# Optimization experiments

Measured on AMD Instinct MI355X. Metric: run time of the kernel, lower is better.

Reference implementation:

```python
import jax, jax.numpy as jnp
import numpy as np

B, A = 1024, 256                 # batch, padded action-space size
N_ENT, N_REL = 100000, 500
E_DIM, R_DIM, H_DIM = 200, 200, 400
ACT_DIM = E_DIM + R_DIM          # action embedding = [rel_emb ; ent_emb]
IN_DIM = E_DIM + H_DIM + R_DIM   # X = cat([E, H, Q])
HUGE = 1e31                      # ops.HUGE_INT
EPS = 1e-20


def setup_inputs() -> dict:
    key = jax.random.key(0)
    ks = jax.random.split(key, 12)
    inp = {
        "e": jax.random.randint(ks[0], (B,), 0, N_ENT),
        "q": jax.random.randint(ks[1], (B,), 0, N_REL),
        "H": jax.random.normal(ks[2], (B, H_DIM), dtype=jnp.float32),
        "r_space": jax.random.randint(ks[3], (B, A), 0, N_REL),
        "e_space": jax.random.randint(ks[4], (B, A), 0, N_ENT),
        "action_mask": jax.random.randint(ks[5], (B, A), 0, 2).astype(jnp.int32),
        # learned parameters
        "entity_emb": jax.random.normal(ks[6], (N_ENT, E_DIM), dtype=jnp.float32) * 0.02,
        "relation_emb": jax.random.normal(ks[7], (N_REL, R_DIM), dtype=jnp.float32) * 0.02,
        "W1": jax.random.normal(ks[8], (IN_DIM, ACT_DIM), dtype=jnp.float32) * (1.0 / np.sqrt(IN_DIM)),
        "b1": jnp.zeros((ACT_DIM,), jnp.float32),
        "W2": jax.random.normal(ks[9], (ACT_DIM, ACT_DIM), dtype=jnp.float32) * (1.0 / np.sqrt(ACT_DIM)),
        "b2": jnp.zeros((ACT_DIM,), jnp.float32),
        "W_att": jax.random.normal(ks[10], (ACT_DIM, R_DIM), dtype=jnp.float32) * (1.0 / np.sqrt(ACT_DIM)),
        "b_att": jnp.zeros((R_DIM,), jnp.float32),
    }
    return inp


def reference(e, q, H, r_space, e_space, action_mask,
              entity_emb, relation_emb, W1, b1, W2, b2, W_att, b_att):
    # state featurization: X = cat([E, H, Q])  -> [B, IN_DIM]
    E = entity_emb[e]
    Q = relation_emb[q]
    X = jnp.concatenate([E, H, Q], axis=-1)
    X = jax.nn.relu(X @ W1 + b1)          # W1 + ReLU (dropout = identity in eval)
    X2 = X @ W2 + b2                      # [B, ACT_DIM]

    # relation attention over all relations
    relation_att = jax.nn.softmax((X2 @ W_att + b_att) @ relation_emb.T, axis=-1)  # [B, N_REL]

    # action embeddings: A = cat([rel_emb[r_space], ent_emb[e_space]])  [B, A, ACT_DIM]
    A_emb = jnp.concatenate([relation_emb[r_space], entity_emb[e_space]], axis=-1)

    mask = action_mask.astype(X2.dtype)
    scores = jnp.einsum('bad,bd->ba', A_emb, X2) - (1.0 - mask) * HUGE
    action_dist = jax.nn.softmax(scores, axis=-1)                      # [B, A]
    entropy = -jnp.sum(action_dist * jnp.log(action_dist + EPS), axis=-1)  # [B]
    return action_dist, entropy, relation_att
```

## Files before the change

### kernel.cpp

```cpp
#include <hip/hip_runtime.h>

#define BATCH   1024
#define ASZ     256
#define EDIM    200
#define RDIM    200
#define HDIM    400
#define ACTDIM  400
#define INDIM   800
#define NRELS   500

typedef __attribute__((ext_vector_type(8))) short short8v;
typedef __attribute__((ext_vector_type(4))) float float4v;
typedef unsigned short u16;

__device__ __forceinline__ u16 f2bf(float f) {
    union { float f; unsigned u; } v; v.f = f;
    unsigned r = v.u + 0x7FFFu + ((v.u >> 16) & 1u);
    return (u16)(r >> 16);
}

template<int ABF, int BBF, int CT, int GAT>
__device__ __forceinline__ void mgemm_body(
    const void* __restrict__ A, const void* __restrict__ B,
    float* __restrict__ Cp, u16* __restrict__ CTout, int ldct,
    int M, int N, int K, int bn, int bm, int z, int nz,
    const int* e_s, const int* q_s,
    const float* __restrict__ Hm, const float* __restrict__ ent,
    const float* __restrict__ rel,
    short* As, short* Bs, int t)
{
    const int tot = (K + 31) >> 5;
    const int s0 = (z * tot) / nz, s1 = ((z + 1) * tot) / nz;

    const int lane = t & 63, w = t >> 6;
    const int l15 = lane & 15, l4 = lane >> 4;
    const int wr = (w >> 1) * 32, wc = (w & 1) * 32;

    const int row = t >> 2;
    const int kc  = (t & 3) * 8;

    float4v acc00 = {0.f,0.f,0.f,0.f}, acc01 = {0.f,0.f,0.f,0.f};
    float4v acc10 = {0.f,0.f,0.f,0.f}, acc11 = {0.f,0.f,0.f,0.f};

    for (int s = s0; s < s1; ++s) {
        const int k0 = s << 5;
        {
            const int gk = k0 + kc;
            __attribute__((aligned(16))) u16 v[8];
            if (GAT) {
                const float* p;
                if (gk < EDIM)            p = ent + (long)e_s[row] * EDIM + gk;
                else if (gk < EDIM+HDIM)  p = Hm  + (long)(bm + row) * HDIM + (gk - EDIM);
                else                      p = rel + (long)q_s[row] * RDIM + (gk - EDIM - HDIM);
                float4 f0 = *(const float4*)p;
                float4 f1 = *(const float4*)(p + 4);
                v[0]=f2bf(f0.x); v[1]=f2bf(f0.y); v[2]=f2bf(f0.z); v[3]=f2bf(f0.w);
                v[4]=f2bf(f1.x); v[5]=f2bf(f1.y); v[6]=f2bf(f1.z); v[7]=f2bf(f1.w);
            } else {
                const int gr = bm + row;
                if (gr < M && gk + 8 <= K) {
                    if (ABF) {
                        *(uint4*)v = *(const uint4*)((const u16*)A + (long)gr * K + gk);
                    } else {
                        const float* p = (const float*)A + (long)gr * K + gk;
                        float4 f0 = *(const float4*)p;
                        float4 f1 = *(const float4*)(p + 4);
                        v[0]=f2bf(f0.x); v[1]=f2bf(f0.y); v[2]=f2bf(f0.z); v[3]=f2bf(f0.w);
                        v[4]=f2bf(f1.x); v[5]=f2bf(f1.y); v[6]=f2bf(f1.z); v[7]=f2bf(f1.w);
                    }
                } else {
#pragma unroll
                    for (int i = 0; i < 8; ++i) v[i] = 0;
                }
            }
            *(uint4*)&As[row * 40 + kc] = *(uint4*)v;
        }
        {
            const int gr = bn + row;
            const int gk = k0 + kc;
            __attribute__((aligned(16))) u16 v[8];
            if (gr < N && gk + 8 <= K) {
                if (BBF) {
                    *(uint4*)v = *(const uint4*)((const u16*)B + (long)gr * K + gk);
                } else {
                    const float* p = (const float*)B + (long)gr * K + gk;
                    float4 f0 = *(const float4*)p;
                    float4 f1 = *(const float4*)(p + 4);
                    v[0]=f2bf(f0.x); v[1]=f2bf(f0.y); v[2]=f2bf(f0.z); v[3]=f2bf(f0.w);
                    v[4]=f2bf(f1.x); v[5]=f2bf(f1.y); v[6]=f2bf(f1.z); v[7]=f2bf(f1.w);
                }
            } else {
#pragma unroll
                for (int i = 0; i < 8; ++i) v[i] = 0;
            }
            *(uint4*)&Bs[row * 40 + kc] = *(uint4*)v;
        }
        __syncthreads();
        short8v a0 = *(short8v*)&As[(wr      + l15) * 40 + l4 * 8];
        short8v a1 = *(short8v*)&As[(wr + 16 + l15) * 40 + l4 * 8];
        short8v b0 = *(short8v*)&Bs[(wc      + l15) * 40 + l4 * 8];
        short8v b1 = *(short8v*)&Bs[(wc + 16 + l15) * 40 + l4 * 8];
        acc00 = __builtin_amdgcn_mfma_f32_16x16x32_bf16(a0, b0, acc00, 0, 0, 0);
        acc01 = __builtin_amdgcn_mfma_f32_16x16x32_bf16(a0, b1, acc01, 0, 0, 0);
        acc10 = __builtin_amdgcn_mfma_f32_16x16x32_bf16(a1, b0, acc10, 0, 0, 0);
        acc11 = __builtin_amdgcn_mfma_f32_16x16x32_bf16(a1, b1, acc11, 0, 0, 0);
        __syncthreads();
    }

    const int rm0 = bm + wr + l4 * 4;
    const int cn0 = bn + wc + l15;
    if (CT == 1) {
        float* dst = Cp + (long)z * M * N;
#pragma unroll
        for (int r = 0; r < 4; ++r) {
            int gm0 = rm0 + r, gm1 = rm0 + 16 + r;
            if (gm0 < M) {
                if (cn0 < N)      dst[(long)gm0 * N + cn0]      = acc00[r];
                if (cn0 + 16 < N) dst[(long)gm0 * N + cn0 + 16] = acc01[r];
            }
            if (gm1 < M) {
                if (cn0 < N)      dst[(long)gm1 * N + cn0]      = acc10[r];
                if (cn0 + 16 < N) dst[(long)gm1 * N + cn0 + 16] = acc11[r];
            }
        }
    } else {
#pragma unroll
        for (int r = 0; r < 4; ++r) {
            int gm0 = rm0 + r, gm1 = rm0 + 16 + r;
            if (gm0 < M) {
                if (cn0 < N)      CTout[(long)cn0 * ldct + gm0]        = f2bf(acc00[r]);
                if (cn0 + 16 < N) CTout[(long)(cn0 + 16) * ldct + gm0] = f2bf(acc01[r]);
            }
            if (gm1 < M) {
                if (cn0 < N)      CTout[(long)cn0 * ldct + gm1]        = f2bf(acc10[r]);
                if (cn0 + 16 < N) CTout[(long)(cn0 + 16) * ldct + gm1] = f2bf(acc11[r]);
            }
        }
    }
}

template<int ABF, int BBF, int CT, int GAT>
__global__ __launch_bounds__(256) void k_mgemm(
    const void* __restrict__ A, const void* __restrict__ B,
    float* __restrict__ Cp, u16* __restrict__ CTout, int ldct,
    int M, int N, int K,
    const int* __restrict__ eidx, const int* __restrict__ qidx,
    const float* __restrict__ Hm, const float* __restrict__ ent,
    const float* __restrict__ rel)
{
    __shared__ __align__(16) short As[64 * 40];
    __shared__ __align__(16) short Bs[64 * 40];
    __shared__ int e_s[64], q_s[64];
    const int t = threadIdx.x;
    const int bm = blockIdx.y * 64;
    if (GAT) {
        if (t < 64) {
            e_s[t] = eidx[bm + t];
            q_s[t] = qidx[bm + t];
        }
        __syncthreads();
    }
    mgemm_body<ABF, BBF, CT, GAT>(A, B, Cp, CTout, ldct, M, N, K,
                                  blockIdx.x * 64, bm, blockIdx.z, gridDim.z,
                                  e_s, q_s, Hm, ent, rel, As, Bs, t);
}

__global__ __launch_bounds__(256) void k_prep_all(
    const float* __restrict__ W1, const float* __restrict__ W2,
    const float* __restrict__ batt, const float* __restrict__ rel,
    const float* __restrict__ Watt,
    u16* __restrict__ W1t, u16* __restrict__ W2t,
    u16* __restrict__ BbigT, float* __restrict__ bbig2)
{
    __shared__ __align__(16) short As[64 * 40];
    __shared__ __align__(16) short Bs[64 * 40];
    __shared__ float tile[32][33];
    __shared__ float bs[200];

    int blk = blockIdx.x, t = threadIdx.x;

    if (blk < 325) {
        int tk = blk / 13, tn = blk % 13;
        int k0 = tk * 32, n0 = tn * 32;
        int i = t >> 3, j4 = (t & 7) * 4;
#pragma unroll
        for (int jj = 0; jj < 4; ++jj) {
            int n = n0 + j4 + jj;
            tile[i][j4 + jj] = (n < 400) ? W1[(long)(k0 + i) * 400 + n] : 0.f;
        }
        __syncthreads();
        int o = t >> 3;
        if (n0 + o < 400) {
            ushort4 u;
            u.x = f2bf(tile[j4 + 0][o]); u.y = f2bf(tile[j4 + 1][o]);
            u.z = f2bf(tile[j4 + 2][o]); u.w = f2bf(tile[j4 + 3][o]);
            *(ushort4*)(W1t + (long)(n0 + o) * 800 + k0 + j4) = u;
        }
    } else if (blk < 494) {
        int idx = blk - 325;
        int tk = idx / 13, tn = idx % 13;
        int k0 = tk * 32, n0 = tn * 32;
        int i = t >> 3, j4 = (t & 7) * 4;
#pragma unroll
        for (int jj = 0; jj < 4; ++jj) {
            int n = n0 + j4 + jj;
            tile[i][j4 + jj] = (k0 + i < 400 && n < 400) ? W2[(long)(k0 + i) * 400 + n] : 0.f;
        }
        __syncthreads();
        int o = t >> 3;
        if (n0 + o < 400) {
#pragma unroll
            for (int jj = 0; jj < 4; ++jj) {
                int k = k0 + j4 + jj;
                if (k < 400) W2t[(long)(n0 + o) * 400 + k] = f2bf(tile[j4 + jj][o]);
            }
        }
    } else if (blk < 594) {
        int gid = (blk - 494) * 256 + t;
        for (int g = gid; g < 50000; g += 100 * 256) {
            int n = g / 100, kq = (g % 100) * 4;
            ushort4 u;
            u.x = (kq + 0 < 200) ? f2bf(rel[(long)n * 200 + kq + 0]) : (u16)0;
            u.y = (kq + 1 < 200) ? f2bf(rel[(long)n * 200 + kq + 1]) : (u16)0;
            u.z = (kq + 2 < 200) ? f2bf(rel[(long)n * 200 + kq + 2]) : (u16)0;
            u.w = (kq + 3 < 200) ? f2bf(rel[(long)n * 200 + kq + 3]) : (u16)0;
            *(ushort4*)(BbigT + (long)(500 + n) * 400 + kq) = u;
        }
    } else if (blk == 594) {
        if (t < 200) bs[t] = batt[t];
        __syncthreads();
        for (int n = t; n < NRELS; n += 256) {
            const float* rr = rel + (long)n * RDIM;
            float s = 0.f;
            for (int k = 0; k < 200; ++k) s += bs[k] * rr[k];
            bbig2[n] = s;
        }
    } else {
        int idx = blk - 595;
        int bn = (idx & 7) * 64, bm = (idx >> 3) * 64;
        mgemm_body<0, 0, 2, 0>(Watt, rel, nullptr, BbigT, 400,
                               400, 500, 200, bn, bm, 0, 1,
                               nullptr, nullptr, nullptr, nullptr, nullptr,
                               As, Bs, t);
    }
}

template<int RELU, int OUT>
__global__ __launch_bounds__(128) void k_reduce2(
    const float* __restrict__ Cp, const float* __restrict__ bias,
    float* __restrict__ Cf, u16* __restrict__ Cb, int M, int N, int nks)
{
    int m = blockIdx.x;
    int nf4 = N >> 2;
    for (int f = threadIdx.x; f < nf4; f += 128) {
        long off = (long)m * N + f * 4;
        float4 s = *(const float4*)(Cp + off);
        for (int ks = 1; ks < nks; ++ks) {
            float4 v = *(const float4*)(Cp + (long)ks * M * N + off);
            s.x += v.x; s.y += v.y; s.z += v.z; s.w += v.w;
        }
        float4 bb = *(const float4*)(bias + f * 4);
        s.x += bb.x; s.y += bb.y; s.z += bb.z; s.w += bb.w;
        if (RELU) {
            s.x = fmaxf(s.x, 0.f); s.y = fmaxf(s.y, 0.f);
            s.z = fmaxf(s.z, 0.f); s.w = fmaxf(s.w, 0.f);
        }
        if (OUT != 1) *(float4*)(Cf + off) = s;
        if (OUT != 0) {
            ushort4 u;
            u.x = f2bf(s.x); u.y = f2bf(s.y); u.z = f2bf(s.z); u.w = f2bf(s.w);
            *(ushort4*)(Cb + off) = u;
        }
    }
}

__global__ __launch_bounds__(512) void k_scores(
    const float* __restrict__ X2, const float* __restrict__ Cp,
    const float* __restrict__ brel,
    const int* __restrict__ r_space, const int* __restrict__ e_space,
    const int* __restrict__ amask,
    const float* __restrict__ ent_emb,
    float* __restrict__ out_dist, float* __restrict__ out_ent,
    float* __restrict__ out_rel)
{
    int b = blockIdx.x, t = threadIdx.x;
    int wave = t >> 6, lane = t & 63;
    __shared__ __align__(16) float4 xt4[50];
    __shared__ float xr[NRELS];
    __shared__ float sc[ASZ];
    __shared__ int   smask[ASZ];
    __shared__ float red[8];

    const float* rowX2 = X2 + (long)b * ACTDIM;
    const float* c0 = Cp + (long)b * 1000;
    const float* c1 = Cp + (long)BATCH * 1000 + (long)b * 1000;
    if (t < 50) xt4[t] = *(const float4*)(rowX2 + 200 + 4 * t);
    for (int i = t; i < NRELS; i += 512) xr[i] = c0[500 + i] + c1[500 + i];

    int abase = wave * 32;
    int r_idx = 0, e_idx = 0, mk = 0;
    if (lane < 32) {
        long base = (long)b * ASZ + abase + lane;
        r_idx = r_space[base];
        e_idx = e_space[base];
        mk    = amask[base];
        smask[abase + lane] = mk;
    }
    __syncthreads();

    float4 x = (lane < 50) ? xt4[lane] : make_float4(0.f, 0.f, 0.f, 0.f);

#pragma unroll
    for (int i = 0; i < 8; ++i) {
        float s[4] = {0.f, 0.f, 0.f, 0.f};
        int rj[4];
#pragma unroll
        for (int j = 0; j < 4; ++j) {
            int a = 4 * i + j;
            int m0 = __shfl(mk, a);
            rj[j]  = __shfl(r_idx, a);
            if (m0) {
                int e0 = __shfl(e_idx, a);
                if (lane < 50) {
                    float4 v = ((const float4*)(ent_emb + (long)e0 * EDIM))[lane];
                    s[j] = v.x * x.x + v.y * x.y + v.z * x.z + v.w * x.w;
                }
            }
        }
#pragma unroll
        for (int off = 32; off > 0; off >>= 1) {
            s[0] += __shfl_xor(s[0], off);
            s[1] += __shfl_xor(s[1], off);
            s[2] += __shfl_xor(s[2], off);
            s[3] += __shfl_xor(s[3], off);
        }
        if (lane == 0) {
            sc[abase + 4 * i + 0] = s[0] + xr[rj[0]];
            sc[abase + 4 * i + 1] = s[1] + xr[rj[1]];
            sc[abase + 4 * i + 2] = s[2] + xr[rj[2]];
            sc[abase + 4 * i + 3] = s[3] + xr[rj[3]];
        }
    }
    __syncthreads();

    float v = -3.4e38f;
    float evv = 0.f;
    if (t < ASZ) v = smask[t] ? sc[t] : -1e31f;

    float m = v;
#pragma unroll
    for (int off = 32; off > 0; off >>= 1) m = fmaxf(m, __shfl_xor(m, off));
    if (t < ASZ && lane == 0) red[wave] = m;
    __syncthreads();
    float mm = fmaxf(fmaxf(red[0], red[1]), fmaxf(red[2], red[3]));
    __syncthreads();

    if (t < ASZ) evv = expf(v - mm);
    float ss = evv;
#pragma unroll
    for (int off = 32; off > 0; off >>= 1) ss += __shfl_xor(ss, off);
    if (t < ASZ && lane == 0) red[wave] = ss;
    __syncthreads();
    float tot = red[0] + red[1] + red[2] + red[3];
    __syncthreads();

    float term = 0.f;
    if (t < ASZ) {
        float p = evv / tot;
        out_dist[(long)b * ASZ + t] = p;
        term = p * logf(p + 1e-20f);
    }
#pragma unroll
    for (int off = 32; off > 0; off >>= 1) term += __shfl_xor(term, off);
    if (t < ASZ && lane == 0) red[wave] = term;
    __syncthreads();
    if (t == 0) out_ent[b] = -(red[0] + red[1] + red[2] + red[3]);
    __syncthreads();

    float rv = (t < NRELS) ? (c0[t] + c1[t] + brel[t]) : -3.4e38f;

    float rm = rv;
#pragma unroll
    for (int off = 32; off > 0; off >>= 1) rm = fmaxf(rm, __shfl_xor(rm, off));
    if (lane == 0) red[wave] = rm;
    __syncthreads();
    rm = fmaxf(fmaxf(fmaxf(red[0], red[1]), fmaxf(red[2], red[3])),
               fmaxf(fmaxf(red[4], red[5]), fmaxf(red[6], red[7])));
    __syncthreads();

    float rev = (t < NRELS) ? expf(rv - rm) : 0.f;
    float rs = rev;
#pragma unroll
    for (int off = 32; off > 0; off >>= 1) rs += __shfl_xor(rs, off);
    if (lane == 0) red[wave] = rs;
    __syncthreads();
    rs = red[0] + red[1] + red[2] + red[3] + red[4] + red[5] + red[6] + red[7];
    if (t < NRELS) out_rel[(long)b * NRELS + t] = rev / rs;
}

extern "C" void kernel_launch(void* const* d_in, const int* in_sizes, int n_in,
                              void* d_out, int out_size, void* d_ws, size_t ws_size,
                              hipStream_t stream)
{
    const int*   e       = (const int*)  d_in[0];
    const int*   q       = (const int*)  d_in[1];
    const float* H       = (const float*)d_in[2];
    const int*   r_space = (const int*)  d_in[3];
    const int*   e_space = (const int*)  d_in[4];
    const int*   amask   = (const int*)  d_in[5];
    const float* ent     = (const float*)d_in[6];
    const float* rel     = (const float*)d_in[7];
    const float* W1      = (const float*)d_in[8];
    const float* b1      = (const float*)d_in[9];
    const float* W2      = (const float*)d_in[10];
    const float* b2      = (const float*)d_in[11];
    const float* Watt    = (const float*)d_in[12];
    const float* batt    = (const float*)d_in[13];

    float* out      = (float*)d_out;
    float* out_dist = out;
    float* out_ent  = out + (long)BATCH * ASZ;
    float* out_rel  = out_ent + BATCH;

    char* ws = (char*)d_ws;
    u16*   X1_bf  = (u16*)  (ws + 0);
    float* X2     = (float*)(ws + 819200);
    u16*   X2_bf  = (u16*)  (ws + 2457600);
    u16*   W1t    = (u16*)  (ws + 3276800);
    u16*   W2t    = (u16*)  (ws + 3916800);
    u16*   BbigT  = (u16*)  (ws + 4236800);
    float* bbig2  = (float*)(ws + 5036800);
    float* Cp     = (float*)(ws + 5242880);

    k_prep_all<<<651, 256, 0, stream>>>(W1, W2, batt, rel, Watt,
                                        W1t, W2t, BbigT, bbig2);

    k_mgemm<1, 1, 1, 1><<<dim3(7, 16, 4), 256, 0, stream>>>(
        nullptr, W1t, Cp, nullptr, 0, BATCH, ACTDIM, INDIM, e, q, H, ent, rel);
    k_reduce2<1, 1><<<BATCH, 128, 0, stream>>>(Cp, b1, nullptr, X1_bf, BATCH, ACTDIM, 4);

    k_mgemm<1, 1, 1, 0><<<dim3(7, 16, 4), 256, 0, stream>>>(
        X1_bf, W2t, Cp, nullptr, 0, BATCH, ACTDIM, ACTDIM,
        nullptr, nullptr, nullptr, nullptr, nullptr);
    k_reduce2<0, 2><<<BATCH, 128, 0, stream>>>(Cp, b2, X2, X2_bf, BATCH, ACTDIM, 4);

    k_mgemm<1, 1, 1, 0><<<dim3(16, 16, 2), 256, 0, stream>>>(
        X2_bf, BbigT, Cp, nullptr, 0, BATCH, 1000, ACTDIM,
        nullptr, nullptr, nullptr, nullptr, nullptr);

    k_scores<<<BATCH, 512, 0, stream>>>(X2, Cp, bbig2, r_space, e_space, amask,
                                        ent, out_dist, out_ent, out_rel);
}
```

Before: 89.55 us.

## Fuse bias epilogue into W2 GEMM, prefetch GEMM tiles, widen score reduction

The second-layer GEMM now runs without split-K and applies bias directly in its epilogue, writing both fp32 and bf16 outputs. This removes the separate partial-sum buffer and the reduce kernel launch. All GEMMs also register-prefetch the next K tile while the current one is being computed, hiding global load latency behind the MFMA work. The scoring kernel processes 8 actions per iteration with a split butterfly reduction to cut shuffle count. The trade-off is that dropping split-K gives the W2 GEMM only 112 blocks, which may underfill the GPU.

```diff
diff --git a/kernel.cpp b/kernel.cpp
--- a/kernel.cpp
+++ b/kernel.cpp
@@ -19,10 +19,11 @@
     return (u16)(r >> 16);
 }
 
-template<int ABF, int BBF, int CT, int GAT>
+template<int ABF, int BBF, int CT, int GAT, int RELU>
 __device__ __forceinline__ void mgemm_body(
     const void* __restrict__ A, const void* __restrict__ B,
     float* __restrict__ Cp, u16* __restrict__ CTout, int ldct,
+    const float* __restrict__ bias, float* __restrict__ Cf, u16* __restrict__ Cb,
     int M, int N, int K, int bn, int bm, int z, int nz,
     const int* e_s, const int* q_s,
     const float* __restrict__ Hm, const float* __restrict__ ent,
@@ -39,63 +40,66 @@
     const int row = t >> 2;
     const int kc  = (t & 3) * 8;
 
+    auto loadA = [&](int s) -> uint4 {
+        const int gk = (s << 5) + kc;
+        __attribute__((aligned(16))) u16 v[8];
+        if (GAT) {
+            const float* p;
+            if (gk < EDIM)              p = ent + (long)e_s[row] * EDIM + gk;
+            else if (gk < EDIM + HDIM)  p = Hm  + (long)(bm + row) * HDIM + (gk - EDIM);
+            else                        p = rel + (long)q_s[row] * RDIM + (gk - EDIM - HDIM);
+            float4 f0 = *(const float4*)p;
+            float4 f1 = *(const float4*)(p + 4);
+            v[0]=f2bf(f0.x); v[1]=f2bf(f0.y); v[2]=f2bf(f0.z); v[3]=f2bf(f0.w);
+            v[4]=f2bf(f1.x); v[5]=f2bf(f1.y); v[6]=f2bf(f1.z); v[7]=f2bf(f1.w);
+            return *(uint4*)v;
+        }
+        const int gr = bm + row;
+        if (gr < M && gk + 8 <= K) {
+            if (ABF) return *(const uint4*)((const u16*)A + (long)gr * K + gk);
+            const float* p = (const float*)A + (long)gr * K + gk;
+            float4 f0 = *(const float4*)p;
+            float4 f1 = *(const float4*)(p + 4);
+            v[0]=f2bf(f0.x); v[1]=f2bf(f0.y); v[2]=f2bf(f0.z); v[3]=f2bf(f0.w);
+            v[4]=f2bf(f1.x); v[5]=f2bf(f1.y); v[6]=f2bf(f1.z); v[7]=f2bf(f1.w);
+            return *(uint4*)v;
+        }
+#pragma unroll
+        for (int i = 0; i < 8; ++i) v[i] = 0;
+        return *(uint4*)v;
+    };
+    auto loadB = [&](int s) -> uint4 {
+        const int gk = (s << 5) + kc;
+        const int gr = bn + row;
+        __attribute__((aligned(16))) u16 v[8];
+        if (gr < N && gk + 8 <= K) {
+            if (BBF) return *(const uint4*)((const u16*)B + (long)gr * K + gk);
+            const float* p = (const float*)B + (long)gr * K + gk;
+            float4 f0 = *(const float4*)p;
+            float4 f1 = *(const float4*)(p + 4);
+            v[0]=f2bf(f0.x); v[1]=f2bf(f0.y); v[2]=f2bf(f0.z); v[3]=f2bf(f0.w);
+            v[4]=f2bf(f1.x); v[5]=f2bf(f1.y); v[6]=f2bf(f1.z); v[7]=f2bf(f1.w);
+            return *(uint4*)v;
+        }
+#pragma unroll
+        for (int i = 0; i < 8; ++i) v[i] = 0;
+        return *(uint4*)v;
+    };
+
     float4v acc00 = {0.f,0.f,0.f,0.f}, acc01 = {0.f,0.f,0.f,0.f};
     float4v acc10 = {0.f,0.f,0.f,0.f}, acc11 = {0.f,0.f,0.f,0.f};
 
+    uint4 ra = loadA(s0);
+    uint4 rb = loadB(s0);
+
     for (int s = s0; s < s1; ++s) {
-        const int k0 = s << 5;
-        {
-            const int gk = k0 + kc;
-            __attribute__((aligned(16))) u16 v[8];
-            if (GAT) {
-                const float* p;
-                if (gk < EDIM)            p = ent + (long)e_s[row] * EDIM + gk;
-                else if (gk < EDIM+HDIM)  p = Hm  + (long)(bm + row) * HDIM + (gk - EDIM);
-                else                      p = rel + (long)q_s[row] * RDIM + (gk - EDIM - HDIM);
-                float4 f0 = *(const float4*)p;
-                float4 f1 = *(const float4*)(p + 4);
-                v[0]=f2bf(f0.x); v[1]=f2bf(f0.y); v[2]=f2bf(f0.z); v[3]=f2bf(f0.w);
-                v[4]=f2bf(f1.x); v[5]=f2bf(f1.y); v[6]=f2bf(f1.z); v[7]=f2bf(f1.w);
-            } else {
-                const int gr = bm + row;
-                if (gr < M && gk + 8 <= K) {
-                    if (ABF) {
-                        *(uint4*)v = *(const uint4*)((const u16*)A + (long)gr * K + gk);
-                    } else {
-                        const float* p = (const float*)A + (long)gr * K + gk;
-                        float4 f0 = *(const float4*)p;
-                        float4 f1 = *(const float4*)(p + 4);
-                        v[0]=f2bf(f0.x); v[1]=f2bf(f0.y); v[2]=f2bf(f0.z); v[3]=f2bf(f0.w);
-                        v[4]=f2bf(f1.x); v[5]=f2bf(f1.y); v[6]=f2bf(f1.z); v[7]=f2bf(f1.w);
-                    }
-                } else {
-#pragma unroll
-                    for (int i = 0; i < 8; ++i) v[i] = 0;
-                }
-            }
-            *(uint4*)&As[row * 40 + kc] = *(uint4*)v;
-        }
-        {
-            const int gr = bn + row;
-            const int gk = k0 + kc;
-            __attribute__((aligned(16))) u16 v[8];
-            if (gr < N && gk + 8 <= K) {
-                if (BBF) {
-                    *(uint4*)v = *(const uint4*)((const u16*)B + (long)gr * K + gk);
-                } else {
-                    const float* p = (const float*)B + (long)gr * K + gk;
-                    float4 f0 = *(const float4*)p;
-                    float4 f1 = *(const float4*)(p + 4);
-                    v[0]=f2bf(f0.x); v[1]=f2bf(f0.y); v[2]=f2bf(f0.z); v[3]=f2bf(f0.w);
-                    v[4]=f2bf(f1.x); v[5]=f2bf(f1.y); v[6]=f2bf(f1.z); v[7]=f2bf(f1.w);
-                }
-            } else {
-#pragma unroll
-                for (int i = 0; i < 8; ++i) v[i] = 0;
-            }
-            *(uint4*)&Bs[row * 40 + kc] = *(uint4*)v;
-        }
+        *(uint4*)&As[row * 40 + kc] = ra;
+        *(uint4*)&Bs[row * 40 + kc] = rb;
         __syncthreads();
+        if (s + 1 < s1) {
+            ra = loadA(s + 1);
+            rb = loadB(s + 1);
+        }
         short8v a0 = *(short8v*)&As[(wr      + l15) * 40 + l4 * 8];
         short8v a1 = *(short8v*)&As[(wr + 16 + l15) * 40 + l4 * 8];
         short8v b0 = *(short8v*)&Bs[(wc      + l15) * 40 + l4 * 8];
@@ -123,7 +127,7 @@
                 if (cn0 + 16 < N) dst[(long)gm1 * N + cn0 + 16] = acc11[r];
             }
         }
-    } else {
+    } else if (CT == 2) {
 #pragma unroll
         for (int r = 0; r < 4; ++r) {
             int gm0 = rm0 + r, gm1 = rm0 + 16 + r;
@@ -136,13 +140,49 @@
                 if (cn0 + 16 < N) CTout[(long)(cn0 + 16) * ldct + gm1] = f2bf(acc11[r]);
             }
         }
-    }
-}
-
-template<int ABF, int BBF, int CT, int GAT>
+    } else {
+        float bv0 = (cn0 < N)      ? bias[cn0]      : 0.f;
+        float bv1 = (cn0 + 16 < N) ? bias[cn0 + 16] : 0.f;
+#pragma unroll
+        for (int r = 0; r < 4; ++r) {
+            int gm0 = rm0 + r, gm1 = rm0 + 16 + r;
+            if (gm0 < M) {
+                if (cn0 < N) {
+                    float v = acc00[r] + bv0;
+                    if (RELU) v = fmaxf(v, 0.f);
+                    Cf[(long)gm0 * N + cn0] = v;
+                    Cb[(long)gm0 * N + cn0] = f2bf(v);
+                }
+                if (cn0 + 16 < N) {
+                    float v = acc01[r] + bv1;
+                    if (RELU) v = fmaxf(v, 0.f);
+                    Cf[(long)gm0 * N + cn0 + 16] = v;
+                    Cb[(long)gm0 * N + cn0 + 16] = f2bf(v);
+                }
+            }
+            if (gm1 < M) {
+                if (cn0 < N) {
+                    float v = acc10[r] + bv0;
+                    if (RELU) v = fmaxf(v, 0.f);
+                    Cf[(long)gm1 * N + cn0] = v;
+                    Cb[(long)gm1 * N + cn0] = f2bf(v);
+                }
+                if (cn0 + 16 < N) {
+                    float v = acc11[r] + bv1;
+                    if (RELU) v = fmaxf(v, 0.f);
+                    Cf[(long)gm1 * N + cn0 + 16] = v;
+                    Cb[(long)gm1 * N + cn0 + 16] = f2bf(v);
+                }
+            }
+        }
+    }
+}
+
+template<int ABF, int BBF, int CT, int GAT, int RELU>
 __global__ __launch_bounds__(256) void k_mgemm(
     const void* __restrict__ A, const void* __restrict__ B,
     float* __restrict__ Cp, u16* __restrict__ CTout, int ldct,
+    const float* __restrict__ bias, float* __restrict__ Cf, u16* __restrict__ Cb,
     int M, int N, int K,
     const int* __restrict__ eidx, const int* __restrict__ qidx,
     const float* __restrict__ Hm, const float* __restrict__ ent,
@@ -160,9 +200,10 @@
         }
         __syncthreads();
     }
-    mgemm_body<ABF, BBF, CT, GAT>(A, B, Cp, CTout, ldct, M, N, K,
-                                  blockIdx.x * 64, bm, blockIdx.z, gridDim.z,
-                                  e_s, q_s, Hm, ent, rel, As, Bs, t);
+    mgemm_body<ABF, BBF, CT, GAT, RELU>(A, B, Cp, CTout, ldct, bias, Cf, Cb,
+                                        M, N, K, blockIdx.x * 64, bm,
+                                        blockIdx.z, gridDim.z,
+                                        e_s, q_s, Hm, ent, rel, As, Bs, t);
 }
 
 __global__ __launch_bounds__(256) void k_prep_all(
@@ -238,10 +279,11 @@
     } else {
         int idx = blk - 595;
         int bn = (idx & 7) * 64, bm = (idx >> 3) * 64;
-        mgemm_body<0, 0, 2, 0>(Watt, rel, nullptr, BbigT, 400,
-                               400, 500, 200, bn, bm, 0, 1,
-                               nullptr, nullptr, nullptr, nullptr, nullptr,
-                               As, Bs, t);
+        mgemm_body<0, 0, 2, 0, 0>(Watt, rel, nullptr, BbigT, 400,
+                                  nullptr, nullptr, nullptr,
+                                  400, 500, 200, bn, bm, 0, 1,
+                                  nullptr, nullptr, nullptr, nullptr, nullptr,
+                                  As, Bs, t);
     }
 }
 
@@ -309,36 +351,42 @@
     __syncthreads();
 
     float4 x = (lane < 50) ? xt4[lane] : make_float4(0.f, 0.f, 0.f, 0.f);
-
-#pragma unroll
-    for (int i = 0; i < 8; ++i) {
-        float s[4] = {0.f, 0.f, 0.f, 0.f};
-        int rj[4];
-#pragma unroll
-        for (int j = 0; j < 4; ++j) {
-            int a = 4 * i + j;
+    const int g = lane >> 4;
+
+#pragma unroll
+    for (int i = 0; i < 4; ++i) {
+        float s[8] = {0.f,0.f,0.f,0.f,0.f,0.f,0.f,0.f};
+        int rj[8];
+#pragma unroll
+        for (int j = 0; j < 8; ++j) {
+            int a = 8 * i + j;
             int m0 = __shfl(mk, a);
             rj[j]  = __shfl(r_idx, a);
             if (m0) {
                 int e0 = __shfl(e_idx, a);
                 if (lane < 50) {
                     float4 v = ((const float4*)(ent_emb + (long)e0 * EDIM))[lane];
-                    s[j] = v.x * x.x + v.y * x.y + v.z * x.z + v.w * x.w;
+                    s[j] = fmaf(v.x, x.x, fmaf(v.y, x.y, fmaf(v.z, x.z, v.w * x.w)));
                 }
             }
         }
 #pragma unroll
-        for (int off = 32; off > 0; off >>= 1) {
-            s[0] += __shfl_xor(s[0], off);
-            s[1] += __shfl_xor(s[1], off);
-            s[2] += __shfl_xor(s[2], off);
-            s[3] += __shfl_xor(s[3], off);
-        }
-        if (lane == 0) {
-            sc[abase + 4 * i + 0] = s[0] + xr[rj[0]];
-            sc[abase + 4 * i + 1] = s[1] + xr[rj[1]];
-            sc[abase + 4 * i + 2] = s[2] + xr[rj[2]];
-            sc[abase + 4 * i + 3] = s[3] + xr[rj[3]];
+        for (int j = 0; j < 8; ++j) {
+            s[j] += __shfl_xor(s[j], 32);
+            s[j] += __shfl_xor(s[j], 16);
+        }
+        float v0 = (g == 0) ? s[0] : (g == 1) ? s[1] : (g == 2) ? s[2] : s[3];
+        float v1 = (g == 0) ? s[4] : (g == 1) ? s[5] : (g == 2) ? s[6] : s[7];
+#pragma unroll
+        for (int off = 8; off > 0; off >>= 1) {
+            v0 += __shfl_xor(v0, off);
+            v1 += __shfl_xor(v1, off);
+        }
+        int r0sel = (g == 0) ? rj[0] : (g == 1) ? rj[1] : (g == 2) ? rj[2] : rj[3];
+        int r1sel = (g == 0) ? rj[4] : (g == 1) ? rj[5] : (g == 2) ? rj[6] : rj[7];
+        if ((lane & 15) == 0) {
+            sc[abase + 8 * i + g]     = v0 + xr[r0sel];
+            sc[abase + 8 * i + 4 + g] = v1 + xr[r1sel];
         }
     }
     __syncthreads();
@@ -435,18 +483,18 @@
     k_prep_all<<<651, 256, 0, stream>>>(W1, W2, batt, rel, Watt,
                                         W1t, W2t, BbigT, bbig2);
 
-    k_mgemm<1, 1, 1, 1><<<dim3(7, 16, 4), 256, 0, stream>>>(
-        nullptr, W1t, Cp, nullptr, 0, BATCH, ACTDIM, INDIM, e, q, H, ent, rel);
+    k_mgemm<1, 1, 1, 1, 0><<<dim3(7, 16, 4), 256, 0, stream>>>(
+        nullptr, W1t, Cp, nullptr, 0, nullptr, nullptr, nullptr,
+        BATCH, ACTDIM, INDIM, e, q, H, ent, rel);
     k_reduce2<1, 1><<<BATCH, 128, 0, stream>>>(Cp, b1, nullptr, X1_bf, BATCH, ACTDIM, 4);
 
-    k_mgemm<1, 1, 1, 0><<<dim3(7, 16, 4), 256, 0, stream>>>(
-        X1_bf, W2t, Cp, nullptr, 0, BATCH, ACTDIM, ACTDIM,
-        nullptr, nullptr, nullptr, nullptr, nullptr);
-    k_reduce2<0, 2><<<BATCH, 128, 0, stream>>>(Cp, b2, X2, X2_bf, BATCH, ACTDIM, 4);
-
-    k_mgemm<1, 1, 1, 0><<<dim3(16, 16, 2), 256, 0, stream>>>(
-        X2_bf, BbigT, Cp, nullptr, 0, BATCH, 1000, ACTDIM,
-        nullptr, nullptr, nullptr, nullptr, nullptr);
+    k_mgemm<1, 1, 3, 0, 0><<<dim3(7, 16, 1), 256, 0, stream>>>(
+        X1_bf, W2t, nullptr, nullptr, 0, b2, X2, X2_bf,
+        BATCH, ACTDIM, ACTDIM, nullptr, nullptr, nullptr, nullptr, nullptr);
+
+    k_mgemm<1, 1, 1, 0, 0><<<dim3(16, 16, 2), 256, 0, stream>>>(
+        X2_bf, BbigT, Cp, nullptr, 0, nullptr, nullptr, nullptr,
+        BATCH, 1000, ACTDIM, nullptr, nullptr, nullptr, nullptr, nullptr);
 
     k_scores<<<BATCH, 512, 0, stream>>>(X2, Cp, bbig2, r_space, e_space, amask,
                                         ent, out_dist, out_ent, out_rel);
```

Result: faster. 80.48 us (-10.1%).
